# Kernel optimization log

Hardware: AMD Instinct MI355X
Metric: run time of the kernel (lower is better)

Reference implementation:

```python
import jax, jax.numpy as jnp
import numpy as np

ALPHA = 0.2  # LeakyReLU negative slope
NEG_INF = -9e15


def setup_inputs() -> dict:
    key = jax.random.key(0)
    ks = jax.random.split(key, 6)
    B, N, F_in, F_out = 16, 1024, 1024, 512
    x = jax.random.normal(ks[0], (B, N, F_in), dtype=jnp.float32)
    adj = jax.random.randint(ks[1], (B, N, N), 0, 2, dtype=jnp.int32)
    W = jax.random.normal(ks[2], (F_in, F_out), dtype=jnp.float32) * 0.02
    a = jax.random.normal(ks[3], (2 * F_out, 1), dtype=jnp.float32) * 0.02
    fc_w = jax.random.normal(ks[4], (F_out, 2 * F_out), dtype=jnp.float32) * 0.02
    fc_b = jnp.zeros((F_out,), dtype=jnp.float32)
    return {"x": x, "adj": adj, "W": W, "a": a, "fc_w": fc_w, "fc_b": fc_b}


def reference(x, adj, W, a, fc_w, fc_b):
    # h: [B, N, F_out]
    h = jnp.matmul(x, W)
    F_out = W.shape[1]
    # The original builds a_input = concat(h_i, h_j) of shape [B,N,N,2F] and
    # contracts with a. Equivalently (same math, no O(N^2 F) intermediate):
    # e_ij = leakyrelu(h_i . a[:F] + h_j . a[F:])
    a1 = a[:F_out, 0]  # [F_out]
    a2 = a[F_out:, 0]  # [F_out]
    f1 = jnp.einsum('bnf,f->bn', h, a1)  # source term
    f2 = jnp.einsum('bnf,f->bn', h, a2)  # target term
    e = jax.nn.leaky_relu(f1[:, :, None] + f2[:, None, :], negative_slope=ALPHA)  # [B,N,N]
    attention = jnp.where(adj > 0, e, jnp.full_like(e, NEG_INF))
    attention = jax.nn.softmax(attention, axis=2)
    # dropout is identity in eval mode
    agg = jnp.matmul(attention, h)  # [B,N,F_out]
    h_prime = jnp.concatenate([agg, h], axis=2)  # [B,N,2F]
    h_prime = jnp.matmul(h_prime, fc_w.T) + fc_b
    return jax.nn.elu(h_prime)  # concat=True path
```

## Files before the change

kernel.cpp:

```cpp
#include <hip/hip_runtime.h>

#define ALPHA 0.2f

typedef __attribute__((ext_vector_type(8))) short short8;
typedef __attribute__((ext_vector_type(4))) float f32x4;

__device__ __forceinline__ unsigned short f2b(float f) {
  unsigned int u; __builtin_memcpy(&u, &f, 4);
  unsigned int r = (u + 0x7FFFu + ((u >> 16) & 1u)) >> 16;
  return (unsigned short)r;
}
__device__ __forceinline__ float b2f(unsigned short v) {
  unsigned int u = ((unsigned int)v) << 16; float f; __builtin_memcpy(&f, &u, 4); return f;
}
__device__ __forceinline__ void gl_lds16(const unsigned short* g, unsigned short* l) {
  __builtin_amdgcn_global_load_lds((__attribute__((address_space(1))) void*)g,
                                   (__attribute__((address_space(3))) void*)l, 16, 0, 0);
}

__device__ __forceinline__ void cvt8(const float* __restrict__ in, unsigned short* __restrict__ out,
                                     unsigned int gid) {
  float4 v0 = ((const float4*)in)[gid * 2];
  float4 v1 = ((const float4*)in)[gid * 2 + 1];
  alignas(16) unsigned short o[8];
  o[0] = f2b(v0.x); o[1] = f2b(v0.y); o[2] = f2b(v0.z); o[3] = f2b(v0.w);
  o[4] = f2b(v1.x); o[5] = f2b(v1.y); o[6] = f2b(v1.z); o[7] = f2b(v1.w);
  ((uint4*)out)[gid] = *(const uint4*)o;
}

__global__ __launch_bounds__(256) void prep1(const int* __restrict__ adj,
                                             unsigned short* __restrict__ bm16,
                                             const float* __restrict__ x,
                                             unsigned short* __restrict__ xb,
                                             const float* __restrict__ fcw,
                                             unsigned short* __restrict__ fcwb,
                                             const float* __restrict__ W,
                                             unsigned short* __restrict__ Wt) {
  __shared__ alignas(16) unsigned short tile[64][72];
  unsigned int bx = blockIdx.x;
  unsigned int tid = threadIdx.x;
  if (bx < 4096u) {
    unsigned int gid = bx * 256 + tid;
    const int4* a4 = (const int4*)adj;
    int4 v0 = a4[gid * 4 + 0];
    int4 v1 = a4[gid * 4 + 1];
    int4 v2 = a4[gid * 4 + 2];
    int4 v3 = a4[gid * 4 + 3];
    unsigned int bits = 0;
    bits |= (v0.x > 0) << 0;  bits |= (v0.y > 0) << 1;  bits |= (v0.z > 0) << 2;  bits |= (v0.w > 0) << 3;
    bits |= (v1.x > 0) << 4;  bits |= (v1.y > 0) << 5;  bits |= (v1.z > 0) << 6;  bits |= (v1.w > 0) << 7;
    bits |= (v2.x > 0) << 8;  bits |= (v2.y > 0) << 9;  bits |= (v2.z > 0) << 10; bits |= (v2.w > 0) << 11;
    bits |= (v3.x > 0) << 12; bits |= (v3.y > 0) << 13; bits |= (v3.z > 0) << 14; bits |= (v3.w > 0) << 15;
    bm16[gid] = (unsigned short)bits;
  } else if (bx < 12288u) {
    cvt8(x, xb, (bx - 4096u) * 256 + tid);
  } else if (bx < 12544u) {
    cvt8(fcw, fcwb, (bx - 12288u) * 256 + tid);
  } else {
    unsigned int idx = bx - 12544u;
    unsigned int k0 = (idx >> 3) * 64, n0 = (idx & 7) * 64;
    #pragma unroll
    for (int p = 0; p < 4; p++) {
      int r = p * 16 + (tid >> 4);
      int c = (tid & 15) * 4;
      float4 v = *(const float4*)(W + (size_t)(k0 + r) * 512 + n0 + c);
      tile[r][c] = f2b(v.x); tile[r][c + 1] = f2b(v.y);
      tile[r][c + 2] = f2b(v.z); tile[r][c + 3] = f2b(v.w);
    }
    __syncthreads();
    int f = tid >> 2;
    int ic = (tid & 3) * 16;
    alignas(16) unsigned short buf[16];
    #pragma unroll
    for (int k = 0; k < 16; k++) buf[k] = tile[ic + k][f];
    uint4* dst = (uint4*)(Wt + (size_t)(n0 + f) * 1024 + k0 + ic);
    dst[0] = ((const uint4*)buf)[0];
    dst[1] = ((const uint4*)buf)[1];
  }
}

__global__ __launch_bounds__(256) void prep2(const unsigned short* __restrict__ hp,
                                             const float* __restrict__ a,
                                             float* __restrict__ f1, float* __restrict__ f2,
                                             unsigned short* __restrict__ ht) {
  __shared__ alignas(16) unsigned short tile[64][72];
  int bx = blockIdx.x;
  int tid = threadIdx.x;
  if (bx < 4096) {
    int row = bx * 4 + (tid >> 6);
    int lane = tid & 63;
    const unsigned short* hrow = hp + (size_t)row * 1024 + 512;
    uint4 raw = *(const uint4*)(hrow + lane * 8);
    alignas(16) unsigned short hv[8]; __builtin_memcpy(hv, &raw, 16);
    float s1 = 0.f, s2 = 0.f;
    #pragma unroll
    for (int j = 0; j < 8; j++) {
      float hf = b2f(hv[j]);
      s1 += hf * a[lane * 8 + j];
      s2 += hf * a[512 + lane * 8 + j];
    }
    #pragma unroll
    for (int o = 32; o > 0; o >>= 1) { s1 += __shfl_down(s1, o); s2 += __shfl_down(s2, o); }
    if (lane == 0) { f1[row] = s1; f2[row] = s2; }
  } else {
    int idx = bx - 4096;
    int b = idx >> 7;
    int f0 = ((idx >> 4) & 7) * 64;
    int i0 = (idx & 15) * 64;
    #pragma unroll
    for (int p = 0; p < 2; p++) {
      int r = p * 32 + (tid >> 3);
      int c = (tid & 7) * 8;
      uint4 v = *(const uint4*)(hp + (size_t)(b * 1024 + i0 + r) * 1024 + 512 + f0 + c);
      *(uint4*)(&tile[r][c]) = v;
    }
    __syncthreads();
    int f = tid >> 2;
    int ic = (tid & 3) * 16;
    alignas(16) unsigned short buf[16];
    #pragma unroll
    for (int k = 0; k < 16; k++) buf[k] = tile[ic + k][f];
    uint4* dst = (uint4*)(ht + (size_t)(b * 512 + f0 + f) * 1024 + i0 + ic);
    dst[0] = ((const uint4*)buf)[0];
    dst[1] = ((const uint4*)buf)[1];
  }
}

__global__ __launch_bounds__(256) void rowsum_P(const unsigned short* __restrict__ bm16,
                                                const float* __restrict__ f1,
                                                const float* __restrict__ f2,
                                                float* __restrict__ invl,
                                                unsigned short* __restrict__ P) {
  int row = blockIdx.x * 4 + (threadIdx.x >> 6);
  int lane = threadIdx.x & 63;
  int b = row >> 10;
  float f1v = f1[row];
  unsigned int bits = bm16[(size_t)row * 64 + lane];
  const float* f2p = f2 + (b << 10) + lane * 16;
  float4 v0 = ((const float4*)f2p)[0];
  float4 v1 = ((const float4*)f2p)[1];
  float4 v2 = ((const float4*)f2p)[2];
  float4 v3 = ((const float4*)f2p)[3];
  float fv[16] = {v0.x, v0.y, v0.z, v0.w, v1.x, v1.y, v1.z, v1.w,
                  v2.x, v2.y, v2.z, v2.w, v3.x, v3.y, v3.z, v3.w};
  float s = 0.f;
  alignas(16) unsigned short o[16];
  #pragma unroll
  for (int j = 0; j < 16; j++) {
    float p = 0.f;
    if ((bits >> j) & 1u) {
      float z = f1v + fv[j];
      z = z > 0.f ? z : ALPHA * z;
      p = __expf(z);
      s += p;
    }
    o[j] = f2b(p);
  }
  uint4* dst = (uint4*)(P + (size_t)row * 1024 + lane * 16);
  dst[0] = ((const uint4*)o)[0];
  dst[1] = ((const uint4*)o)[1];
  #pragma unroll
  for (int off = 32; off > 0; off >>= 1) s += __shfl_down(s, off);
  if (lane == 0) invl[row] = 1.0f / s;
}

template <int EPI>
__global__ __launch_bounds__(256) void gemm_bt(
    const unsigned short* __restrict__ A, size_t aBS,
    const unsigned short* __restrict__ Bt, size_t bBS,
    int K,
    void* __restrict__ outp, size_t oBS, int ldo, int ocol,
    const float* __restrict__ scale,
    const float* __restrict__ bias) {
  __shared__ alignas(16) unsigned short As[128 * 64];
  __shared__ alignas(16) unsigned short Bs[128 * 64];
  const int tid = threadIdx.x;
  const int lane = tid & 63;
  const int w = tid >> 6;
  const int m0 = blockIdx.x * 128;
  const int n0 = blockIdx.y * 128;
  const int zb = blockIdx.z;
  const unsigned short* Ab = A + (size_t)zb * aBS;
  const unsigned short* Btb = Bt + (size_t)zb * bBS;

  f32x4 acc[4][4];
  #pragma unroll
  for (int i = 0; i < 4; i++)
    #pragma unroll
    for (int j = 0; j < 4; j++)
      #pragma unroll
      for (int r = 0; r < 4; r++) acc[i][j][r] = 0.f;

  const int lr = lane >> 3;
  const int lc = (lane & 7) ^ (lr & 7);
  const unsigned short* ag = Ab + (size_t)(m0 + w * 32 + lr) * K + lc * 8;
  const unsigned short* bg = Btb + (size_t)(n0 + w * 32 + lr) * K + lc * 8;
  unsigned short* asl = As + w * 32 * 64;
  unsigned short* bsl = Bs + w * 32 * 64;

  const int wm = (w & 1) * 64;
  const int wn = (w >> 1) * 64;
  const int row16 = lane & 15;
  const int quad = lane >> 4;
  const int sw = row16 & 7;

  for (int k0 = 0; k0 < K; k0 += 64) {
    __syncthreads();
    #pragma unroll
    for (int t = 0; t < 4; t++) {
      gl_lds16(ag + k0 + (size_t)(t * 8) * K, asl + t * 512);
      gl_lds16(bg + k0 + (size_t)(t * 8) * K, bsl + t * 512);
    }
    __syncthreads();
    short8 af[2][4], bf[2][4];
    #pragma unroll
    for (int s = 0; s < 2; s++) {
      #pragma unroll
      for (int i = 0; i < 4; i++) {
        af[s][i] = *(const short8*)(As + (wm + i * 16 + row16) * 64 + ((s * 4 + quad) ^ sw) * 8);
        bf[s][i] = *(const short8*)(Bs + (wn + i * 16 + row16) * 64 + ((s * 4 + quad) ^ sw) * 8);
      }
    }
    #pragma unroll
    for (int s = 0; s < 2; s++)
      #pragma unroll
      for (int am = 0; am < 4; am++)
        #pragma unroll
        for (int bn = 0; bn < 4; bn++)
          acc[am][bn] = __builtin_amdgcn_mfma_f32_16x16x32_bf16(af[s][am], bf[s][bn], acc[am][bn], 0, 0, 0);
  }

  const int col = lane & 15;
  const int r0 = quad * 4;
  #pragma unroll
  for (int am = 0; am < 4; am++) {
    #pragma unroll
    for (int bn = 0; bn < 4; bn++) {
      #pragma unroll
      for (int r = 0; r < 4; r++) {
        int m = m0 + wm + am * 16 + r0 + r;
        int n = n0 + wn + bn * 16 + col;
        float v = acc[am][bn][r];
        if (EPI == 3) v *= scale[zb * 1024 + m];
        if (EPI == 2) {
          v += bias[n];
          v = v > 0.f ? v : expm1f(v);
          ((float*)outp)[(size_t)m * ldo + n] = v;
        } else {
          ((unsigned short*)outp)[(size_t)zb * oBS + (size_t)m * ldo + ocol + n] = f2b(v);
        }
      }
    }
  }
}

extern "C" void kernel_launch(void* const* d_in, const int* in_sizes, int n_in,
                              void* d_out, int out_size, void* d_ws, size_t ws_size,
                              hipStream_t stream) {
  const float* x   = (const float*)d_in[0];
  const int*   adj = (const int*)d_in[1];
  const float* W   = (const float*)d_in[2];
  const float* a   = (const float*)d_in[3];
  const float* fcw = (const float*)d_in[4];
  const float* fcb = (const float*)d_in[5];
  float* out = (float*)d_out;
  char* ws = (char*)d_ws;

  unsigned short* xb   = (unsigned short*)(ws);
  unsigned short* hp   = (unsigned short*)(ws + 33554432);
  unsigned short* ht   = (unsigned short*)(ws + 67108864);
  unsigned short* Wt   = (unsigned short*)(ws + 83886080);
  unsigned short* fcwb = (unsigned short*)(ws + 84934656);
  float* f1            = (float*)(ws + 85983232);
  float* f2            = (float*)(ws + 86048768);
  float* invl          = (float*)(ws + 86114304);
  unsigned short* bm   = (unsigned short*)(ws + 86179840);
  unsigned short* P = xb;

  prep1<<<12672, 256, 0, stream>>>(adj, bm, x, xb, fcw, fcwb, W, Wt);

  gemm_bt<1><<<dim3(128, 4, 1), 256, 0, stream>>>(xb, 0, Wt, 0, 1024,
                                                  hp, 0, 1024, 512, nullptr, nullptr);
  prep2<<<6144, 256, 0, stream>>>(hp, a, f1, f2, ht);
  rowsum_P<<<4096, 256, 0, stream>>>(bm, f1, f2, invl, P);

  gemm_bt<3><<<dim3(8, 4, 16), 256, 0, stream>>>(P, 1024 * 1024, ht, 512 * 1024, 1024,
                                                 hp, 1024 * 1024, 1024, 0, invl, nullptr);
  gemm_bt<2><<<dim3(128, 4, 1), 256, 0, stream>>>(hp, 0, fcwb, 0, 1024,
                                                  out, 0, 512, 0, nullptr, fcb);
}
```

Measured before the change: 266.1 us.

## Restructure GEMM to 8 waves with 32x32x16 MFMA and K-step 32

The bf16 GEMM kernel moves from 4 waves using 16x16x32 MFMA with a K-step of 64 to 8 waves (512 threads) using 32x32x16 MFMA with a K-step of 32. Each wave now computes a 64x32 sub-tile with two 16-float accumulators, and LDS tiles shrink to 128x32 with no XOR swizzle. The aim is lower register pressure, more waves to hide latency, and the larger MFMA shape. In exchange the loop runs twice as many iterations with two barriers each, and the unswizzled LDS reads may hit bank conflicts.

```diff
diff --git a/kernel.cpp b/kernel.cpp
--- a/kernel.cpp
+++ b/kernel.cpp
@@ -3,7 +3,7 @@
 #define ALPHA 0.2f
 
 typedef __attribute__((ext_vector_type(8))) short short8;
-typedef __attribute__((ext_vector_type(4))) float f32x4;
+typedef __attribute__((ext_vector_type(16))) float f32x16;
 
 __device__ __forceinline__ unsigned short f2b(float f) {
   unsigned int u; __builtin_memcpy(&u, &f, 4);
@@ -165,15 +165,15 @@
 }
 
 template <int EPI>
-__global__ __launch_bounds__(256) void gemm_bt(
+__global__ __launch_bounds__(512, 4) void gemm_bt(
     const unsigned short* __restrict__ A, size_t aBS,
     const unsigned short* __restrict__ Bt, size_t bBS,
     int K,
     void* __restrict__ outp, size_t oBS, int ldo, int ocol,
     const float* __restrict__ scale,
     const float* __restrict__ bias) {
-  __shared__ alignas(16) unsigned short As[128 * 64];
-  __shared__ alignas(16) unsigned short Bs[128 * 64];
+  __shared__ alignas(16) unsigned short As[128 * 32];
+  __shared__ alignas(16) unsigned short Bs[128 * 32];
   const int tid = threadIdx.x;
   const int lane = tid & 63;
   const int w = tid >> 6;
@@ -183,72 +183,56 @@
   const unsigned short* Ab = A + (size_t)zb * aBS;
   const unsigned short* Btb = Bt + (size_t)zb * bBS;
 
-  f32x4 acc[4][4];
-  #pragma unroll
-  for (int i = 0; i < 4; i++)
-    #pragma unroll
-    for (int j = 0; j < 4; j++)
-      #pragma unroll
-      for (int r = 0; r < 4; r++) acc[i][j][r] = 0.f;
-
-  const int lr = lane >> 3;
-  const int lc = (lane & 7) ^ (lr & 7);
-  const unsigned short* ag = Ab + (size_t)(m0 + w * 32 + lr) * K + lc * 8;
-  const unsigned short* bg = Btb + (size_t)(n0 + w * 32 + lr) * K + lc * 8;
-  unsigned short* asl = As + w * 32 * 64;
-  unsigned short* bsl = Bs + w * 32 * 64;
+  f32x16 acc[2];
+  #pragma unroll
+  for (int t = 0; t < 2; t++)
+    #pragma unroll
+    for (int r = 0; r < 16; r++) acc[t][r] = 0.f;
+
+  const int sr = w * 16 + (lane >> 2);
+  const int sc = (lane & 3) * 8;
+  const unsigned short* ag = Ab + (size_t)(m0 + sr) * K + sc;
+  const unsigned short* bg = Btb + (size_t)(n0 + sr) * K + sc;
+  unsigned short* asl = As + w * 512;
+  unsigned short* bsl = Bs + w * 512;
 
   const int wm = (w & 1) * 64;
-  const int wn = (w >> 1) * 64;
-  const int row16 = lane & 15;
-  const int quad = lane >> 4;
-  const int sw = row16 & 7;
-
-  for (int k0 = 0; k0 < K; k0 += 64) {
-    __syncthreads();
-    #pragma unroll
-    for (int t = 0; t < 4; t++) {
-      gl_lds16(ag + k0 + (size_t)(t * 8) * K, asl + t * 512);
-      gl_lds16(bg + k0 + (size_t)(t * 8) * K, bsl + t * 512);
-    }
-    __syncthreads();
-    short8 af[2][4], bf[2][4];
+  const int wn = (w >> 1) * 32;
+  const int l31 = lane & 31;
+  const int kh = lane >> 5;
+
+  for (int k0 = 0; k0 < K; k0 += 32) {
+    __syncthreads();
+    gl_lds16(ag + k0, asl);
+    gl_lds16(bg + k0, bsl);
+    __syncthreads();
     #pragma unroll
     for (int s = 0; s < 2; s++) {
-      #pragma unroll
-      for (int i = 0; i < 4; i++) {
-        af[s][i] = *(const short8*)(As + (wm + i * 16 + row16) * 64 + ((s * 4 + quad) ^ sw) * 8);
-        bf[s][i] = *(const short8*)(Bs + (wn + i * 16 + row16) * 64 + ((s * 4 + quad) ^ sw) * 8);
-      }
-    }
-    #pragma unroll
-    for (int s = 0; s < 2; s++)
-      #pragma unroll
-      for (int am = 0; am < 4; am++)
-        #pragma unroll
-        for (int bn = 0; bn < 4; bn++)
-          acc[am][bn] = __builtin_amdgcn_mfma_f32_16x16x32_bf16(af[s][am], bf[s][bn], acc[am][bn], 0, 0, 0);
-  }
-
-  const int col = lane & 15;
-  const int r0 = quad * 4;
-  #pragma unroll
-  for (int am = 0; am < 4; am++) {
-    #pragma unroll
-    for (int bn = 0; bn < 4; bn++) {
-      #pragma unroll
-      for (int r = 0; r < 4; r++) {
-        int m = m0 + wm + am * 16 + r0 + r;
-        int n = n0 + wn + bn * 16 + col;
-        float v = acc[am][bn][r];
-        if (EPI == 3) v *= scale[zb * 1024 + m];
-        if (EPI == 2) {
-          v += bias[n];
-          v = v > 0.f ? v : expm1f(v);
-          ((float*)outp)[(size_t)m * ldo + n] = v;
-        } else {
-          ((unsigned short*)outp)[(size_t)zb * oBS + (size_t)m * ldo + ocol + n] = f2b(v);
-        }
+      short8 af0 = *(const short8*)(As + (wm + l31) * 32 + (s * 2 + kh) * 8);
+      short8 af1 = *(const short8*)(As + (wm + 32 + l31) * 32 + (s * 2 + kh) * 8);
+      short8 bf  = *(const short8*)(Bs + (wn + l31) * 32 + (s * 2 + kh) * 8);
+      acc[0] = __builtin_amdgcn_mfma_f32_32x32x16_bf16(af0, bf, acc[0], 0, 0, 0);
+      acc[1] = __builtin_amdgcn_mfma_f32_32x32x16_bf16(af1, bf, acc[1], 0, 0, 0);
+    }
+  }
+
+  const int col = l31;
+  const int rbase = kh * 4;
+  #pragma unroll
+  for (int t = 0; t < 2; t++) {
+    #pragma unroll
+    for (int r = 0; r < 16; r++) {
+      int row = (r & 3) + 8 * (r >> 2) + rbase;
+      int m = m0 + wm + t * 32 + row;
+      int n = n0 + wn + col;
+      float v = acc[t][r];
+      if (EPI == 3) v *= scale[zb * 1024 + m];
+      if (EPI == 2) {
+        v += bias[n];
+        v = v > 0.f ? v : expm1f(v);
+        ((float*)outp)[(size_t)m * ldo + n] = v;
+      } else {
+        ((unsigned short*)outp)[(size_t)zb * oBS + (size_t)m * ldo + ocol + n] = f2b(v);
       }
     }
   }
@@ -279,13 +263,13 @@
 
   prep1<<<12672, 256, 0, stream>>>(adj, bm, x, xb, fcw, fcwb, W, Wt);
 
-  gemm_bt<1><<<dim3(128, 4, 1), 256, 0, stream>>>(xb, 0, Wt, 0, 1024,
+  gemm_bt<1><<<dim3(128, 4, 1), 512, 0, stream>>>(xb, 0, Wt, 0, 1024,
                                                   hp, 0, 1024, 512, nullptr, nullptr);
   prep2<<<6144, 256, 0, stream>>>(hp, a, f1, f2, ht);
   rowsum_P<<<4096, 256, 0, stream>>>(bm, f1, f2, invl, P);
 
-  gemm_bt<3><<<dim3(8, 4, 16), 256, 0, stream>>>(P, 1024 * 1024, ht, 512 * 1024, 1024,
+  gemm_bt<3><<<dim3(8, 4, 16), 512, 0, stream>>>(P, 1024 * 1024, ht, 512 * 1024, 1024,
                                                  hp, 1024 * 1024, 1024, 0, invl, nullptr);
-  gemm_bt<2><<<dim3(128, 4, 1), 256, 0, stream>>>(hp, 0, fcwb, 0, 1024,
+  gemm_bt<2><<<dim3(128, 4, 1), 512, 0, stream>>>(hp, 0, fcwb, 0, 1024,
                                                   out, 0, 512, 0, nullptr, fcb);
 }
```

Result: slower. 287.0 us (+7.8%).

## Shrink GEMM K-tile to 32, unswizzle LDS, and reorganize prep kernels per-wave

Applied to the files above, without the earlier changes.

The GEMM K-step drops from 64 to 32, halving LDS tiles and removing the XOR swizzle. Rows now load as four 16-byte chunks, which likely brings back LDS bank conflicts and doubles the number of barriers per K. The adjacency bitmask is built per wave with shuffles, one row per wave, and the fp32-to-bf16 conversion writes 8-byte stores with coalesced lane mapping. It also adds an unused, incorrect pack4 helper that returns 0. The aim is lower LDS use and higher occupancy, plus better-coalesced prep loads.

```diff
diff --git a/kernel.cpp b/kernel.cpp
--- a/kernel.cpp
+++ b/kernel.cpp
@@ -17,15 +17,26 @@
   __builtin_amdgcn_global_load_lds((__attribute__((address_space(1))) void*)g,
                                    (__attribute__((address_space(3))) void*)l, 16, 0, 0);
 }
-
-__device__ __forceinline__ void cvt8(const float* __restrict__ in, unsigned short* __restrict__ out,
-                                     unsigned int gid) {
-  float4 v0 = ((const float4*)in)[gid * 2];
-  float4 v1 = ((const float4*)in)[gid * 2 + 1];
-  alignas(16) unsigned short o[8];
-  o[0] = f2b(v0.x); o[1] = f2b(v0.y); o[2] = f2b(v0.z); o[3] = f2b(v0.w);
-  o[4] = f2b(v1.x); o[5] = f2b(v1.y); o[6] = f2b(v1.z); o[7] = f2b(v1.w);
-  ((uint4*)out)[gid] = *(const uint4*)o;
+__device__ __forceinline__ unsigned int pack4(float4 v) {
+  alignas(8) unsigned short o[4];
+  o[0] = f2b(v.x); o[1] = f2b(v.y); o[2] = f2b(v.z); o[3] = f2b(v.w);
+  unsigned long long r = *(const unsigned long long*)o;
+  return 0;
+}
+
+__device__ __forceinline__ void cvt_wave(const float* __restrict__ in,
+                                         unsigned short* __restrict__ out,
+                                         unsigned int wave, unsigned int lane) {
+  const float4* in4 = (const float4*)in;
+  uint2* out2 = (uint2*)out;
+  unsigned int b = wave * 128;
+  float4 v0 = in4[b + lane];
+  float4 v1 = in4[b + 64 + lane];
+  alignas(8) unsigned short o0[4], o1[4];
+  o0[0] = f2b(v0.x); o0[1] = f2b(v0.y); o0[2] = f2b(v0.z); o0[3] = f2b(v0.w);
+  o1[0] = f2b(v1.x); o1[1] = f2b(v1.y); o1[2] = f2b(v1.z); o1[3] = f2b(v1.w);
+  out2[b + lane] = *(const uint2*)o0;
+  out2[b + 64 + lane] = *(const uint2*)o1;
 }
 
 __global__ __launch_bounds__(256) void prep1(const int* __restrict__ adj,
@@ -39,23 +50,25 @@
   __shared__ alignas(16) unsigned short tile[64][72];
   unsigned int bx = blockIdx.x;
   unsigned int tid = threadIdx.x;
+  unsigned int lane = tid & 63;
   if (bx < 4096u) {
-    unsigned int gid = bx * 256 + tid;
-    const int4* a4 = (const int4*)adj;
-    int4 v0 = a4[gid * 4 + 0];
-    int4 v1 = a4[gid * 4 + 1];
-    int4 v2 = a4[gid * 4 + 2];
-    int4 v3 = a4[gid * 4 + 3];
-    unsigned int bits = 0;
-    bits |= (v0.x > 0) << 0;  bits |= (v0.y > 0) << 1;  bits |= (v0.z > 0) << 2;  bits |= (v0.w > 0) << 3;
-    bits |= (v1.x > 0) << 4;  bits |= (v1.y > 0) << 5;  bits |= (v1.z > 0) << 6;  bits |= (v1.w > 0) << 7;
-    bits |= (v2.x > 0) << 8;  bits |= (v2.y > 0) << 9;  bits |= (v2.z > 0) << 10; bits |= (v2.w > 0) << 11;
-    bits |= (v3.x > 0) << 12; bits |= (v3.y > 0) << 13; bits |= (v3.z > 0) << 14; bits |= (v3.w > 0) << 15;
-    bm16[gid] = (unsigned short)bits;
+    unsigned int row = bx * 4 + (tid >> 6);
+    const int4* a4 = (const int4*)adj + (size_t)row * 256;
+    unsigned int g = lane >> 2;
+    unsigned int sh = (lane & 3) * 4;
+    #pragma unroll
+    for (int k = 0; k < 4; k++) {
+      int4 v = a4[k * 64 + lane];
+      unsigned int n = ((v.x > 0) | ((v.y > 0) << 1) | ((v.z > 0) << 2) | ((v.w > 0) << 3)) << sh;
+      n |= __shfl_xor(n, 1);
+      n |= __shfl_xor(n, 2);
+      if ((lane & 3) == 0)
+        bm16[(size_t)row * 64 + k * 16 + g] = (unsigned short)n;
+    }
   } else if (bx < 12288u) {
-    cvt8(x, xb, (bx - 4096u) * 256 + tid);
+    cvt_wave(x, xb, (bx - 4096u) * 4 + (tid >> 6), lane);
   } else if (bx < 12544u) {
-    cvt8(fcw, fcwb, (bx - 12288u) * 256 + tid);
+    cvt_wave(fcw, fcwb, (bx - 12288u) * 4 + (tid >> 6), lane);
   } else {
     unsigned int idx = bx - 12544u;
     unsigned int k0 = (idx >> 3) * 64, n0 = (idx & 7) * 64;
@@ -172,8 +185,8 @@
     void* __restrict__ outp, size_t oBS, int ldo, int ocol,
     const float* __restrict__ scale,
     const float* __restrict__ bias) {
-  __shared__ alignas(16) unsigned short As[128 * 64];
-  __shared__ alignas(16) unsigned short Bs[128 * 64];
+  __shared__ alignas(16) unsigned short As[128 * 32];
+  __shared__ alignas(16) unsigned short Bs[128 * 32];
   const int tid = threadIdx.x;
   const int lane = tid & 63;
   const int w = tid >> 6;
@@ -191,43 +204,37 @@
       #pragma unroll
       for (int r = 0; r < 4; r++) acc[i][j][r] = 0.f;
 
-  const int lr = lane >> 3;
-  const int lc = (lane & 7) ^ (lr & 7);
-  const unsigned short* ag = Ab + (size_t)(m0 + w * 32 + lr) * K + lc * 8;
-  const unsigned short* bg = Btb + (size_t)(n0 + w * 32 + lr) * K + lc * 8;
-  unsigned short* asl = As + w * 32 * 64;
-  unsigned short* bsl = Bs + w * 32 * 64;
+  const int sr = w * 32 + (lane >> 2);
+  const int sc = (lane & 3) * 8;
+  const unsigned short* ag = Ab + (size_t)(m0 + sr) * K + sc;
+  const unsigned short* bg = Btb + (size_t)(n0 + sr) * K + sc;
+  unsigned short* asl = As + w * 1024;
+  unsigned short* bsl = Bs + w * 1024;
 
   const int wm = (w & 1) * 64;
   const int wn = (w >> 1) * 64;
   const int row16 = lane & 15;
   const int quad = lane >> 4;
-  const int sw = row16 & 7;
-
-  for (int k0 = 0; k0 < K; k0 += 64) {
-    __syncthreads();
-    #pragma unroll
-    for (int t = 0; t < 4; t++) {
-      gl_lds16(ag + k0 + (size_t)(t * 8) * K, asl + t * 512);
-      gl_lds16(bg + k0 + (size_t)(t * 8) * K, bsl + t * 512);
-    }
-    __syncthreads();
-    short8 af[2][4], bf[2][4];
-    #pragma unroll
-    for (int s = 0; s < 2; s++) {
+
+  for (int k0 = 0; k0 < K; k0 += 32) {
+    __syncthreads();
+    gl_lds16(ag + k0, asl);
+    gl_lds16(ag + k0 + (size_t)16 * K, asl + 512);
+    gl_lds16(bg + k0, bsl);
+    gl_lds16(bg + k0 + (size_t)16 * K, bsl + 512);
+    __syncthreads();
+    short8 af[4], bf[4];
+    #pragma unroll
+    for (int am = 0; am < 4; am++)
+      af[am] = *(const short8*)(As + (wm + am * 16 + row16) * 32 + quad * 8);
+    #pragma unroll
+    for (int bn = 0; bn < 4; bn++)
+      bf[bn] = *(const short8*)(Bs + (wn + bn * 16 + row16) * 32 + quad * 8);
+    #pragma unroll
+    for (int am = 0; am < 4; am++)
       #pragma unroll
-      for (int i = 0; i < 4; i++) {
-        af[s][i] = *(const short8*)(As + (wm + i * 16 + row16) * 64 + ((s * 4 + quad) ^ sw) * 8);
-        bf[s][i] = *(const short8*)(Bs + (wn + i * 16 + row16) * 64 + ((s * 4 + quad) ^ sw) * 8);
-      }
-    }
-    #pragma unroll
-    for (int s = 0; s < 2; s++)
-      #pragma unroll
-      for (int am = 0; am < 4; am++)
-        #pragma unroll
-        for (int bn = 0; bn < 4; bn++)
-          acc[am][bn] = __builtin_amdgcn_mfma_f32_16x16x32_bf16(af[s][am], bf[s][bn], acc[am][bn], 0, 0, 0);
+      for (int bn = 0; bn < 4; bn++)
+        acc[am][bn] = __builtin_amdgcn_mfma_f32_16x16x32_bf16(af[am], bf[bn], acc[am][bn], 0, 0, 0);
   }
 
   const int col = lane & 15;
```

Result: slower. 283.1 us (+6.4%).
